# Kernel tuning notes

Measured on AMD Instinct MI355X. Metric: run time of the kernel, lower is better.

## Reference

```python
import jax, jax.numpy as jnp
import numpy as np

B, T, D, H = 2, 2048, 2048, 32
d = D // H  # head_dim = 64


def setup_inputs() -> dict:
    key = jax.random.key(0)
    ks = jax.random.split(key, 6)
    s = 2 ** (-2.5) * (2.0 / (D + D)) ** 0.5  # xavier_uniform-ish scale, gain 2^-2.5
    return {
        "hidden_states": jax.random.normal(ks[0], (B, T, D), jnp.float32),
        "Wq": jax.random.normal(ks[1], (D, D), jnp.float32) * s,
        "Wk": jax.random.normal(ks[2], (D, D), jnp.float32) * s,
        "Wv": jax.random.normal(ks[3], (D, D), jnp.float32) * s,
        "Wbeta": jax.random.normal(ks[4], (D, H), jnp.float32) * s,
        "b_beta": jnp.zeros((H,), jnp.float32),
        "Wo": jax.random.normal(ks[5], (D, D), jnp.float32) * s,
    }


def _l2norm(x):
    return x * jax.lax.rsqrt(jnp.sum(x * x, axis=-1, keepdims=True) + 1e-6)


def _parallel_hope(q, k, v, beta):
    """Householder delta-rule linear attention.
    q,k,v: [B,H,T,d]; beta: [B,H,T].
    Recurrence: S_t = S_{t-1} (I - beta_t k_t k_t^T) + beta_t k_t v_t^T  (k l2-normalized,
    so the update is a generalized Householder transform), o_t = q_t^T S_t.
    """
    q = _l2norm(q)
    k = _l2norm(k)

    def step(S, inp):
        q_t, k_t, v_t, b_t = inp  # [B,H,d], [B,H,d], [B,H,d], [B,H]
        # delta rule: new value replaces old prediction, gated by beta
        pred = jnp.einsum('bhk,bhkv->bhv', k_t, S)
        delta = (v_t - pred) * b_t[..., None]
        S = S + jnp.einsum('bhk,bhv->bhkv', k_t, delta)
        o_t = jnp.einsum('bhk,bhkv->bhv', q_t, S)
        return S, o_t

    S0 = jnp.zeros(q.shape[:2] + (q.shape[-1], v.shape[-1]), q.dtype)  # [B,H,d,d]
    xs = (jnp.moveaxis(q, 2, 0), jnp.moveaxis(k, 2, 0),
          jnp.moveaxis(v, 2, 0), jnp.moveaxis(beta, 2, 0))
    _, o = jax.lax.scan(step, S0, xs)  # [T,B,H,d]
    return jnp.moveaxis(o, 0, 2)  # [B,H,T,d]


def reference(hidden_states, Wq, Wk, Wv, Wbeta, b_beta, Wo):
    q = hidden_states @ Wq
    k = hidden_states @ Wk
    v = hidden_states @ Wv
    beta = jax.nn.sigmoid(hidden_states @ Wbeta + b_beta)  # [B,T,H]
    to_heads = lambda x: jnp.moveaxis(x.reshape(B, T, H, d), 1, 2)  # [B,H,T,d]
    q, k, v = to_heads(q), to_heads(k), to_heads(v)
    beta = jnp.moveaxis(beta, 1, 2)  # [B,H,T]
    o = _parallel_hope(q, k, v, beta)  # [B,H,T,d]
    o = jnp.moveaxis(o, 1, 2).reshape(B, T, D)
    return o @ Wo
```

## Files before the change

### kernel.cpp

```cpp
#include <hip/hip_runtime.h>
#include <hip/hip_bf16.h>

typedef __hip_bfloat16 bf16;
typedef __attribute__((ext_vector_type(8))) short short8;
typedef __attribute__((ext_vector_type(4))) float f32x4;

#define NB 2
#define NT 2048
#define ND 2048
#define NH 32
#define NM (NB*NT)
#define NCH 32

__global__ void detect_dtype(const unsigned short* __restrict__ hs, int* __restrict__ flag) {
  if (threadIdx.x == 0 && blockIdx.x == 0) {
    int cnt = 0;
    for (int i = 0; i < 2048; i += 2) {
      int e = (hs[i] >> 7) & 0xFF;
      if (e >= 141) ++cnt;
    }
    *flag = (cnt > 64) ? 1 : 0;
  }
}

__device__ __forceinline__ float loadf(const void* p, size_t i, int isf32) {
  return isf32 ? ((const float*)p)[i] : __bfloat162float(((const bf16*)p)[i]);
}

__global__ __launch_bounds__(256) void convert_bf16(const void* __restrict__ src,
                                                    bf16* __restrict__ dst,
                                                    long n, const int* __restrict__ flag) {
  const long i0 = ((long)blockIdx.x * 256 + threadIdx.x) * 8;
  if (i0 >= n) return;
  if (*flag) {
    const float* s = (const float*)src;
    #pragma unroll
    for (int j = 0; j < 8; ++j) dst[i0 + j] = __float2bfloat16(s[i0 + j]);
  } else {
    *(short8*)(dst + i0) = *(const short8*)((const bf16*)src + i0);
  }
}

__global__ __launch_bounds__(256) void transpose_cvt(const void* __restrict__ src,
                                                     bf16* __restrict__ dst,
                                                     int src_rows, int src_cols,
                                                     const int* __restrict__ flag) {
  __shared__ bf16 tile[64][65];
  const int f = *flag;
  const int tb_r = blockIdx.y * 64, tb_c = blockIdx.x * 64;
  const int tx = threadIdx.x & 63, ty = threadIdx.x >> 6;
  #pragma unroll
  for (int i = 0; i < 64; i += 4) {
    const int cc = tb_c + tx;
    tile[i + ty][tx] = (cc < src_cols)
      ? __float2bfloat16(loadf(src, (size_t)(tb_r + i + ty) * src_cols + cc, f))
      : __float2bfloat16(0.f);
  }
  __syncthreads();
  #pragma unroll
  for (int i = 0; i < 64; i += 4)
    dst[(size_t)(tb_c + i + ty) * src_rows + tb_r + tx] = tile[tx][i + ty];
}

__global__ __launch_bounds__(256) void transpose_qkvb(const void* __restrict__ Wq,
                                                      const void* __restrict__ Wk,
                                                      const void* __restrict__ Wv,
                                                      const void* __restrict__ Wb,
                                                      bf16* __restrict__ WT,
                                                      const int* __restrict__ flag) {
  __shared__ bf16 tile[64][65];
  const int z = blockIdx.z;
  if (z == 3 && blockIdx.x >= 2) return;
  const void* src = (z == 0) ? Wq : (z == 1) ? Wk : (z == 2) ? Wv : Wb;
  const int src_cols = (z == 3) ? 32 : 2048;
  bf16* dst = WT + (size_t)z * 2048 * 2048;
  const int f = *flag;
  const int tb_r = blockIdx.y * 64, tb_c = blockIdx.x * 64;
  const int tx = threadIdx.x & 63, ty = threadIdx.x >> 6;
  #pragma unroll
  for (int i = 0; i < 64; i += 4) {
    const int cc = tb_c + tx;
    tile[i + ty][tx] = (cc < src_cols)
      ? __float2bfloat16(loadf(src, (size_t)(tb_r + i + ty) * src_cols + cc, f))
      : __float2bfloat16(0.f);
  }
  __syncthreads();
  #pragma unroll
  for (int i = 0; i < 64; i += 4)
    dst[(size_t)(tb_c + i + ty) * 2048 + tb_r + tx] = tile[tx][i + ty];
}

__device__ __forceinline__ void gload_lds16(const void* g, void* l) {
  __builtin_amdgcn_global_load_lds((__attribute__((address_space(1))) const void*)g,
                                   (__attribute__((address_space(3))) void*)l,
                                   16, 0, 0);
}

__global__ __launch_bounds__(256) void gemm_bt(const bf16* __restrict__ A,
                                               const bf16* __restrict__ Bt,
                                               bf16* __restrict__ oq, bf16* __restrict__ ok2,
                                               bf16* __restrict__ ov, bf16* __restrict__ ob,
                                               void* __restrict__ outv,
                                               const int* __restrict__ outflag,
                                               int M, int K, int n_base) {
  __shared__ bf16 As[128 * 32];
  __shared__ bf16 Bs[128 * 32];
  const int tid = threadIdx.x;
  const int wave = tid >> 6, lane = tid & 63;
  const int m0 = blockIdx.y * 128, n0 = blockIdx.x * 128;
  const int wm = (wave >> 1) * 64, wn = (wave & 1) * 64;
  const int srow = lane >> 2, scol = (lane & 3) * 8;
  const int frow = lane & 15, fk = (lane >> 4) * 8;
  f32x4 acc[4][4] = {};

  for (int kb = 0; kb < K; kb += 32) {
    __syncthreads();
    #pragma unroll
    for (int j = 0; j < 2; ++j) {
      const int rbase = wave * 32 + j * 16;
      gload_lds16(A  + (size_t)(m0 + rbase + srow) * K + kb + scol, As + rbase * 32);
      gload_lds16(Bt + (size_t)(n0 + rbase + srow) * K + kb + scol, Bs + rbase * 32);
    }
    __syncthreads();
    short8 af[4], bfr[4];
    #pragma unroll
    for (int i = 0; i < 4; ++i)
      af[i] = *(const short8*)(As + (wm + i * 16 + frow) * 32 + fk);
    #pragma unroll
    for (int i = 0; i < 4; ++i)
      bfr[i] = *(const short8*)(Bs + (wn + i * 16 + frow) * 32 + fk);
    #pragma unroll
    for (int mi = 0; mi < 4; ++mi)
      #pragma unroll
      for (int ni = 0; ni < 4; ++ni)
        acc[mi][ni] = __builtin_amdgcn_mfma_f32_16x16x32_bf16(af[mi], bfr[ni], acc[mi][ni], 0, 0, 0);
  }

  const int crow = (lane >> 4) * 4, ccol = lane & 15;
  const int gn0 = n_base + n0;
  if (outflag) {
    const int f = *outflag;
    #pragma unroll
    for (int mi = 0; mi < 4; ++mi)
      #pragma unroll
      for (int ni = 0; ni < 4; ++ni)
        #pragma unroll
        for (int r = 0; r < 4; ++r) {
          const size_t idx = (size_t)(m0 + wm + mi * 16 + crow + r) * 2048 + gn0 + wn + ni * 16 + ccol;
          const float val = acc[mi][ni][r];
          if (f == 1) ((float*)outv)[idx] = val;
          else        ((bf16*)outv)[idx] = __float2bfloat16(val);
        }
  } else {
    const int seg = gn0 >> 11;
    bf16* o = (seg == 0) ? oq : (seg == 1) ? ok2 : (seg == 2) ? ov : ob;
    const int stride = (seg < 3) ? 2048 : 128;
    const int cb = (gn0 & 2047) + wn;
    if (seg <= 1) {
      #pragma unroll
      for (int mi = 0; mi < 4; ++mi)
        #pragma unroll
        for (int r = 0; r < 4; ++r) {
          float s = acc[mi][0][r] * acc[mi][0][r] + acc[mi][1][r] * acc[mi][1][r]
                  + acc[mi][2][r] * acc[mi][2][r] + acc[mi][3][r] * acc[mi][3][r];
          s += __shfl_xor(s, 1, 64); s += __shfl_xor(s, 2, 64);
          s += __shfl_xor(s, 4, 64); s += __shfl_xor(s, 8, 64);
          const float inv = rsqrtf(s + 1e-6f);
          #pragma unroll
          for (int ni = 0; ni < 4; ++ni) acc[mi][ni][r] *= inv;
        }
    }
    #pragma unroll
    for (int mi = 0; mi < 4; ++mi)
      #pragma unroll
      for (int ni = 0; ni < 4; ++ni)
        #pragma unroll
        for (int r = 0; r < 4; ++r)
          o[(size_t)(m0 + wm + mi * 16 + crow + r) * stride + cb + ni * 16 + ccol] =
            __float2bfloat16(acc[mi][ni][r]);
  }
}


template<int TB>
__device__ __forceinline__ void scan16(const float* __restrict__ Af,
                                       const bf16* __restrict__ vsrc,
                                       const float* __restrict__ Bsc,
                                       float (&u)[64], const int lane, const int wave,
                                       const float sgn,
                                       bf16* __restrict__ outT,
                                       bf16* __restrict__ gout) {
  constexpr int JM = (TB + 1) * 16;
  #pragma unroll
  for (int tt = 0; tt < 16; ++tt) {
    const int t = TB * 16 + tt;
    float pr0 = 0.f, pr1 = 0.f, pr2 = 0.f, pr3 = 0.f;
    #pragma unroll
    for (int i = 0; i < JM; i += 4) {
      const f32x4 a = *(const f32x4*)(Af + t * 64 + i);
      pr0 = __builtin_fmaf(a[0], u[i + 0], pr0);
      pr1 = __builtin_fmaf(a[1], u[i + 1], pr1);
      pr2 = __builtin_fmaf(a[2], u[i + 2], pr2);
      pr3 = __builtin_fmaf(a[3], u[i + 3], pr3);
    }
    const float ut = Bsc[t] * __bfloat162float(vsrc[t * 72 + lane])
                   - ((pr0 + pr1) + (pr2 + pr3));
    u[t] = ut;
    const bf16 sv = __float2bfloat16(sgn * ut);
    outT[lane * 72 + t] = sv;
    if (wave) gout[t * 64 + lane] = sv;
  }
}

__global__ __launch_bounds__(256) void chunk_scan(const bf16* __restrict__ k16,
                                                  bf16* __restrict__ v16,
                                                  const bf16* __restrict__ betab,
                                                  const void* __restrict__ bb,
                                                  const int* __restrict__ flag,
                                                  bf16* __restrict__ Gneg,
                                                  bf16* __restrict__ AcT,
                                                  bf16* __restrict__ Dc) {
  __shared__ bf16 Ks[64 * 72];
  __shared__ bf16 Vs[64 * 72];
  __shared__ bf16 GsT[64 * 72];
  __shared__ bf16 UsT[64 * 72];
  __shared__ float Af[64 * 64];
  __shared__ float Bsc[64];
  bf16* const KTs = (bf16*)Af;
  const int ch = blockIdx.x;
  const int c = ch & (NCH - 1), bh = ch >> 5;
  const int h = bh & (NH - 1), b = bh >> 5;
  const int tid = threadIdx.x, wave = tid >> 6, lane = tid & 63;
  const size_t rowb = ((size_t)b * NT + c * 64) * ND + (size_t)h * 64;

  short8 ktA0, ktB0, ktA1, ktB1;
  if (wave >= 2) {
    const int d0a = (wave - 2) * 16, d0b = d0a + 32;
    ktA0 = *(const short8*)(k16 + rowb + (size_t)lane * ND + d0a);
    ktB0 = *(const short8*)(k16 + rowb + (size_t)lane * ND + d0a + 8);
    ktA1 = *(const short8*)(k16 + rowb + (size_t)lane * ND + d0b);
    ktB1 = *(const short8*)(k16 + rowb + (size_t)lane * ND + d0b + 8);
  }
  {
    const int r0 = tid >> 3, sc = (tid & 7) * 8;
    #pragma unroll
    for (int rnd = 0; rnd < 2; ++rnd) {
      const int r = rnd * 32 + r0;
      *(short8*)(Ks + r * 72 + sc) = *(const short8*)(k16 + rowb + (size_t)r * ND + sc);
      *(short8*)(Vs + r * 72 + sc) = *(const short8*)(v16 + rowb + (size_t)r * ND + sc);
    }
  }
  if (tid < 64) {
    const float x = __bfloat162float(betab[((size_t)b * NT + c * 64 + tid) * 128 + h])
                    + loadf(bb, h, *flag);
    Bsc[tid] = 1.f / (1.f + expf(-x));
  }
  __syncthreads();

  const int frow = lane & 15, fk = (lane >> 4) * 8, cm = (lane >> 4) * 4;
  {
    short8 ma0 = *(const short8*)(Ks + (16 * wave + frow) * 72 + fk);
    short8 ma1 = *(const short8*)(Ks + (16 * wave + frow) * 72 + 32 + fk);
    #pragma unroll
    for (int n = 0; n < 4; ++n) {
      f32x4 m = {};
      m = __builtin_amdgcn_mfma_f32_16x16x32_bf16(ma0, *(const short8*)(Ks + (16 * n + frow) * 72 + fk), m, 0, 0, 0);
      m = __builtin_amdgcn_mfma_f32_16x16x32_bf16(ma1, *(const short8*)(Ks + (16 * n + frow) * 72 + 32 + fk), m, 0, 0, 0);
      #pragma unroll
      for (int r = 0; r < 4; ++r) {
        const int t = 16 * wave + cm + r, s = 16 * n + frow;
        Af[t * 64 + s] = (s < t) ? Bsc[t] * m[r] : 0.f;
      }
    }
  }
  __syncthreads();

  if (wave < 2) {
    float u[64];
    #pragma unroll
    for (int i = 0; i < 64; ++i) u[i] = 0.f;
    const bf16* vsrc = wave ? Ks : Vs;
    bf16* outT = wave ? GsT : UsT;
    bf16* gout = Gneg + (size_t)ch * 4096;
    const float sgn = wave ? -1.f : 1.f;
    scan16<0>(Af, vsrc, Bsc, u, lane, wave, sgn, outT, gout);
    scan16<1>(Af, vsrc, Bsc, u, lane, wave, sgn, outT, gout);
    scan16<2>(Af, vsrc, Bsc, u, lane, wave, sgn, outT, gout);
    scan16<3>(Af, vsrc, Bsc, u, lane, wave, sgn, outT, gout);
  }
  __syncthreads();

  if (wave >= 2) {
    const int d0a = (wave - 2) * 16, d0b = d0a + 32;
    #pragma unroll
    for (int j = 0; j < 8; ++j) {
      KTs[(d0a + j) * 72 + lane]     = ((const bf16*)&ktA0)[j];
      KTs[(d0a + 8 + j) * 72 + lane] = ((const bf16*)&ktB0)[j];
      KTs[(d0b + j) * 72 + lane]     = ((const bf16*)&ktA1)[j];
      KTs[(d0b + 8 + j) * 72 + lane] = ((const bf16*)&ktB1)[j];
    }
  }
  __syncthreads();

  short8 ka0 = *(const short8*)(KTs + (16 * wave + frow) * 72 + fk);
  short8 ka1 = *(const short8*)(KTs + (16 * wave + frow) * 72 + 32 + fk);
  short8 uu0 = *(const short8*)(UsT + (16 * wave + frow) * 72 + fk);
  short8 uu1 = *(const short8*)(UsT + (16 * wave + frow) * 72 + 32 + fk);
  #pragma unroll
  for (int n = 0; n < 4; ++n) {
    f32x4 aA = {}, aD = {};
    aA = __builtin_amdgcn_mfma_f32_16x16x32_bf16(ka0, *(const short8*)(GsT + (16 * n + frow) * 72 + fk), aA, 0, 0, 0);
    aA = __builtin_amdgcn_mfma_f32_16x16x32_bf16(ka1, *(const short8*)(GsT + (16 * n + frow) * 72 + 32 + fk), aA, 0, 0, 0);
    aD = __builtin_amdgcn_mfma_f32_16x16x32_bf16(uu0, *(const short8*)(KTs + (16 * n + frow) * 72 + fk), aD, 0, 0, 0);
    aD = __builtin_amdgcn_mfma_f32_16x16x32_bf16(uu1, *(const short8*)(KTs + (16 * n + frow) * 72 + 32 + fk), aD, 0, 0, 0);
    #pragma unroll
    for (int r = 0; r < 4; ++r) {
      Vs[(16 * wave + cm + r) * 64 + 16 * n + frow] = __float2bfloat16(aA[r]);
      Ks[(16 * wave + cm + r) * 64 + 16 * n + frow] = __float2bfloat16(aD[r]);
    }
  }
  __syncthreads();
  {
    const int r0 = tid >> 2, sc2 = (tid & 3) * 16;
    bf16* acg = AcT + (size_t)ch * 4096;
    bf16* dcg = Dc  + (size_t)ch * 4096;
    *(short8*)(acg + r0 * 64 + sc2)     = *(const short8*)(Vs + r0 * 64 + sc2);
    *(short8*)(acg + r0 * 64 + sc2 + 8) = *(const short8*)(Vs + r0 * 64 + sc2 + 8);
    *(short8*)(dcg + r0 * 64 + sc2)     = *(const short8*)(Ks + r0 * 64 + sc2);
    *(short8*)(dcg + r0 * 64 + sc2 + 8) = *(const short8*)(Ks + r0 * 64 + sc2 + 8);
    *(short8*)(v16 + rowb + (size_t)r0 * ND + sc2)     = *(const short8*)(UsT + r0 * 72 + sc2);
    *(short8*)(v16 + rowb + (size_t)r0 * ND + sc2 + 8) = *(const short8*)(UsT + r0 * 72 + sc2 + 8);
  }
}

__global__ __launch_bounds__(256) void state_seq(const bf16* __restrict__ AcT,
                                                 const bf16* __restrict__ Dc,
                                                 bf16* __restrict__ Sbuf) {
  __shared__ bf16 ST[64 * 72];
  const int bh = blockIdx.x;
  const int wave = threadIdx.x >> 6, lane = threadIdx.x & 63;
  const int frow = lane & 15, fk = (lane >> 4) * 8, cm = (lane >> 4) * 4;
  for (int i = threadIdx.x; i < 64 * 72 / 2; i += 256) ((unsigned int*)ST)[i] = 0u;
  f32x4 sacc[4] = {};
  const bf16* ac = AcT + (size_t)bh * NCH * 4096;
  const bf16* dc = Dc  + (size_t)bh * NCH * 4096;
  bf16* sb = Sbuf + (size_t)bh * NCH * 4096;
  #pragma unroll
  for (int n = 0; n < 4; ++n)
    #pragma unroll
    for (int r = 0; r < 4; ++r)
      sb[(16 * wave + cm + r) * 64 + 16 * n + frow] = __float2bfloat16(0.f);
  short8 bpre[4][2];
  float dpre[16];
  #pragma unroll
  for (int n = 0; n < 4; ++n) {
    bpre[n][0] = *(const short8*)(ac + (16 * n + frow) * 64 + fk);
    bpre[n][1] = *(const short8*)(ac + (16 * n + frow) * 64 + 32 + fk);
    #pragma unroll
    for (int r = 0; r < 4; ++r)
      dpre[n * 4 + r] = __bfloat162float(dc[(16 * wave + cm + r) * 64 + 16 * n + frow]);
  }
  __syncthreads();
  #pragma unroll 1
  for (int c = 0; c < NCH; ++c) {
    short8 a0 = *(const short8*)(ST + (16 * wave + frow) * 72 + fk);
    short8 a1 = *(const short8*)(ST + (16 * wave + frow) * 72 + 32 + fk);
    short8 bcur[4][2];
    float dcur[16];
    #pragma unroll
    for (int n = 0; n < 4; ++n) {
      bcur[n][0] = bpre[n][0]; bcur[n][1] = bpre[n][1];
      #pragma unroll
      for (int r = 0; r < 4; ++r) dcur[n * 4 + r] = dpre[n * 4 + r];
    }
    if (c + 1 < NCH) {
      const bf16* acn = ac + (size_t)(c + 1) * 4096;
      const bf16* dcn = dc + (size_t)(c + 1) * 4096;
      #pragma unroll
      for (int n = 0; n < 4; ++n) {
        bpre[n][0] = *(const short8*)(acn + (16 * n + frow) * 64 + fk);
        bpre[n][1] = *(const short8*)(acn + (16 * n + frow) * 64 + 32 + fk);
        #pragma unroll
        for (int r = 0; r < 4; ++r)
          dpre[n * 4 + r] = __bfloat162float(dcn[(16 * wave + cm + r) * 64 + 16 * n + frow]);
      }
    }
    #pragma unroll
    for (int n = 0; n < 4; ++n) {
      sacc[n] = __builtin_amdgcn_mfma_f32_16x16x32_bf16(a0, bcur[n][0], sacc[n], 0, 0, 0);
      sacc[n] = __builtin_amdgcn_mfma_f32_16x16x32_bf16(a1, bcur[n][1], sacc[n], 0, 0, 0);
      #pragma unroll
      for (int r = 0; r < 4; ++r) sacc[n][r] += dcur[n * 4 + r];
    }
    __syncthreads();
    #pragma unroll
    for (int n = 0; n < 4; ++n)
      #pragma unroll
      for (int r = 0; r < 4; ++r) {
        const bf16 sv = __float2bfloat16(sacc[n][r]);
        ST[(16 * wave + cm + r) * 72 + 16 * n + frow] = sv;
        if (c + 1 < NCH)
          sb[(size_t)(c + 1) * 4096 + (16 * wave + cm + r) * 64 + 16 * n + frow] = sv;
      }
    __syncthreads();
  }
}

__global__ __launch_bounds__(256) void chunk_out(bf16* __restrict__ q16,
                                                 const bf16* __restrict__ k16,
                                                 const bf16* __restrict__ v16,
                                                 const bf16* __restrict__ Gneg,
                                                 const bf16* __restrict__ Sbuf) {
  __shared__ bf16 UTs[64 * 72];
  __shared__ bf16 Pt[64 * 72];
  const int ch = blockIdx.x;
  const int c = ch & (NCH - 1), bh = ch >> 5;
  const int h = bh & (NH - 1), b = bh >> 5;
  const int tid = threadIdx.x, wave = tid >> 6, lane = tid & 63;
  const int frow = lane & 15, fk = (lane >> 4) * 8, cm = (lane >> 4) * 4;
  const size_t qkb = ((size_t)b * NT + c * 64) * ND + (size_t)h * 64;
  const bf16* Sb = Sbuf + (size_t)ch * 4096;
  const bf16* Gc = Gneg + (size_t)ch * 4096;
  {
    const int r0 = tid >> 2, sc2 = (tid & 3) * 16;
    *(short8*)(UTs + r0 * 72 + sc2)     = *(const short8*)(v16 + qkb + (size_t)r0 * ND + sc2);
    *(short8*)(UTs + r0 * 72 + sc2 + 8) = *(const short8*)(v16 + qkb + (size_t)r0 * ND + sc2 + 8);
  }
  short8 qa0 = *(const short8*)(q16 + qkb + (size_t)(16 * wave + frow) * ND + fk);
  short8 qa1 = *(const short8*)(q16 + qkb + (size_t)(16 * wave + frow) * ND + 32 + fk);
  f32x4 pacc[4];
  #pragma unroll
  for (int n = 0; n < 4; ++n) {
    f32x4 a = {};
    a = __builtin_amdgcn_mfma_f32_16x16x32_bf16(qa0, *(const short8*)(k16 + qkb + (size_t)(16 * n + frow) * ND + fk), a, 0, 0, 0);
    a = __builtin_amdgcn_mfma_f32_16x16x32_bf16(qa1, *(const short8*)(k16 + qkb + (size_t)(16 * n + frow) * ND + 32 + fk), a, 0, 0, 0);
    pacc[n] = a;
  }
  __syncthreads();
  f32x4 uacc[4];
  #pragma unroll
  for (int n = 0; n < 4; ++n)
    #pragma unroll
    for (int r = 0; r < 4; ++r)
      uacc[n][r] = __bfloat162float(UTs[(16 * wave + cm + r) * 72 + 16 * n + frow]);
  #pragma unroll
  for (int n = 0; n < 4; ++n)
    #pragma unroll
    for (int r = 0; r < 4; ++r) {
      const int mg = 16 * wave + cm + r, ng = 16 * n + frow;
      Pt[mg * 72 + ng] = __float2bfloat16(ng <= mg ? pacc[n][r] : 0.f);
    }
  short8 sa0 = *(const short8*)(Sb + (16 * wave + frow) * 64 + fk);
  short8 sa1 = *(const short8*)(Sb + (16 * wave + frow) * 64 + 32 + fk);
  #pragma unroll
  for (int n = 0; n < 4; ++n) {
    uacc[n] = __builtin_amdgcn_mfma_f32_16x16x32_bf16(sa0, *(const short8*)(Gc + (16 * n + frow) * 64 + fk), uacc[n], 0, 0, 0);
    uacc[n] = __builtin_amdgcn_mfma_f32_16x16x32_bf16(sa1, *(const short8*)(Gc + (16 * n + frow) * 64 + 32 + fk), uacc[n], 0, 0, 0);
  }
  __syncthreads();
  #pragma unroll
  for (int n = 0; n < 4; ++n)
    #pragma unroll
    for (int r = 0; r < 4; ++r)
      UTs[(16 * wave + cm + r) * 72 + 16 * n + frow] = __float2bfloat16(uacc[n][r]);
  __syncthreads();
  short8 pa0 = *(const short8*)(Pt + (16 * wave + frow) * 72 + fk);
  short8 pa1 = *(const short8*)(Pt + (16 * wave + frow) * 72 + 32 + fk);
  #pragma unroll
  for (int n = 0; n < 4; ++n) {
    f32x4 o = {};
    o = __builtin_amdgcn_mfma_f32_16x16x32_bf16(qa0, *(const short8*)(Sb + (16 * n + frow) * 64 + fk), o, 0, 0, 0);
    o = __builtin_amdgcn_mfma_f32_16x16x32_bf16(qa1, *(const short8*)(Sb + (16 * n + frow) * 64 + 32 + fk), o, 0, 0, 0);
    o = __builtin_amdgcn_mfma_f32_16x16x32_bf16(pa0, *(const short8*)(UTs + (16 * n + frow) * 72 + fk), o, 0, 0, 0);
    o = __builtin_amdgcn_mfma_f32_16x16x32_bf16(pa1, *(const short8*)(UTs + (16 * n + frow) * 72 + 32 + fk), o, 0, 0, 0);
    #pragma unroll
    for (int r = 0; r < 4; ++r)
      q16[qkb + (size_t)(16 * wave + cm + r) * ND + 16 * n + frow] = __float2bfloat16(o[r]);
  }
}


__global__ __launch_bounds__(128) void chunk_scan_c(const bf16* __restrict__ k16,
                                                    bf16* __restrict__ v16,
                                                    const bf16* __restrict__ betab,
                                                    const void* __restrict__ bb,
                                                    const int* __restrict__ flag,
                                                    bf16* __restrict__ Gneg) {
  __shared__ bf16 Ks[64 * 64];
  __shared__ bf16 Vs[64 * 64];
  __shared__ bf16 Gs[64 * 64];
  __shared__ float Bs[64];
  const int ch = blockIdx.x;
  const int c = ch & (NCH - 1), bh = ch >> 5;
  const int h = bh & (NH - 1), b = bh >> 5;
  const int tid = threadIdx.x;
  const int wave = tid >> 6, lane = tid & 63;
  const size_t rowb = ((size_t)b * NT + c * 64) * ND + (size_t)h * 64;
  const int sr = tid >> 3, sc = (tid & 7) * 8;
  #pragma unroll
  for (int rnd = 0; rnd < 4; ++rnd) {
    const int r = rnd * 16 + sr;
    *(short8*)(Ks + r * 64 + sc) = *(const short8*)(k16 + rowb + (size_t)r * ND + sc);
    *(short8*)(Vs + r * 64 + sc) = *(const short8*)(v16 + rowb + (size_t)r * ND + sc);
  }
  if (tid < 64) {
    const float x = __bfloat162float(betab[((size_t)b * NT + c * 64 + tid) * 128 + h])
                    + loadf(bb, h, *flag);
    Bs[tid] = 1.f / (1.f + expf(-x));
  }
  __syncthreads();
  float S[64];
  #pragma unroll
  for (int i = 0; i < 64; ++i) S[i] = 0.f;
  const bf16* val_src = wave ? Ks : Vs;
  #pragma unroll 1
  for (int t = 0; t < 64; ++t) {
    uint4 ku[8];
    #pragma unroll
    for (int i = 0; i < 8; ++i) ku[i] = ((const uint4*)(Ks + t * 64))[i];
    const float val = __bfloat162float(val_src[t * 64 + lane]);
    const float bt = Bs[t];
    float kvf[64];
    #pragma unroll
    for (int i = 0; i < 8; ++i) {
      kvf[8*i+0] = __uint_as_float(ku[i].x << 16);
      kvf[8*i+1] = __uint_as_float(ku[i].x & 0xffff0000u);
      kvf[8*i+2] = __uint_as_float(ku[i].y << 16);
      kvf[8*i+3] = __uint_as_float(ku[i].y & 0xffff0000u);
      kvf[8*i+4] = __uint_as_float(ku[i].z << 16);
      kvf[8*i+5] = __uint_as_float(ku[i].z & 0xffff0000u);
      kvf[8*i+6] = __uint_as_float(ku[i].w << 16);
      kvf[8*i+7] = __uint_as_float(ku[i].w & 0xffff0000u);
    }
    float p0 = 0, p1 = 0, p2 = 0, p3 = 0;
    #pragma unroll
    for (int i = 0; i < 16; ++i) {
      p0 += kvf[4*i+0] * S[4*i+0];
      p1 += kvf[4*i+1] * S[4*i+1];
      p2 += kvf[4*i+2] * S[4*i+2];
      p3 += kvf[4*i+3] * S[4*i+3];
    }
    const float u = bt * (val - ((p0 + p1) + (p2 + p3)));
    #pragma unroll
    for (int i = 0; i < 16; ++i) {
      S[4*i+0] += kvf[4*i+0] * u;
      S[4*i+1] += kvf[4*i+1] * u;
      S[4*i+2] += kvf[4*i+2] * u;
      S[4*i+3] += kvf[4*i+3] * u;
    }
    if (wave) Gs[t * 64 + lane] = __float2bfloat16(-u);
    else      Vs[t * 64 + lane] = __float2bfloat16(u);
  }
  __syncthreads();
  bf16* gout = Gneg + (size_t)ch * 4096;
  #pragma unroll
  for (int rnd = 0; rnd < 4; ++rnd) {
    const int r = rnd * 16 + sr;
    *(short8*)(v16 + rowb + (size_t)r * ND + sc) = *(const short8*)(Vs + r * 64 + sc);
    *(short8*)(gout + r * 64 + sc)               = *(const short8*)(Gs + r * 64 + sc);
  }
}

__global__ __launch_bounds__(256) void chunk_seq_mono(bf16* q16,
                                                      const bf16* __restrict__ k16,
                                                      const bf16* __restrict__ Ul,
                                                      const bf16* __restrict__ Gneg) {
  __shared__ bf16 ST[64 * 72];
  __shared__ bf16 Ubt[64 * 72];
  __shared__ bf16 Pt[64 * 72];
  __shared__ bf16 KTl[64 * 72];
  const int bh = blockIdx.x, h = bh & (NH - 1), b = bh >> 5;
  const int wave = threadIdx.x >> 6, lane = threadIdx.x & 63;
  const int frow = lane & 15, q4 = lane >> 4, fk = q4 * 8;
  const int cm = q4 * 4;
  for (int i = threadIdx.x; i < 64 * 72 / 2; i += 256) ((unsigned int*)ST)[i] = 0u;
  __syncthreads();
  f32x4 sacc[4] = {};
  #pragma unroll 1
  for (int c = 0; c < NCH; ++c) {
    const bf16* Gc = Gneg + ((size_t)bh * NCH + c) * 4096;
    const size_t qkb = ((size_t)b * NT + c * 64) * ND + (size_t)h * 64;
    {
      short8 r0 = *(const short8*)(k16 + qkb + (size_t)lane * ND + 16 * wave);
      short8 r1 = *(const short8*)(k16 + qkb + (size_t)lane * ND + 16 * wave + 8);
      #pragma unroll
      for (int j = 0; j < 8; ++j) {
        KTl[(16 * wave + j) * 72 + lane]     = ((const bf16*)&r0)[j];
        KTl[(16 * wave + 8 + j) * 72 + lane] = ((const bf16*)&r1)[j];
      }
    }
    short8 ga0 = *(const short8*)(Gc + (16 * wave + frow) * 64 + fk);
    short8 ga1 = *(const short8*)(Gc + (16 * wave + frow) * 64 + 32 + fk);
    #pragma unroll
    for (int n = 0; n < 4; ++n) {
      f32x4 acc;
      #pragma unroll
      for (int r = 0; r < 4; ++r)
        acc[r] = __bfloat162float(Ul[qkb + (size_t)(16 * wave + cm + r) * ND + 16 * n + frow]);
      acc = __builtin_amdgcn_mfma_f32_16x16x32_bf16(ga0, *(const short8*)(ST + (16 * n + frow) * 72 + fk), acc, 0, 0, 0);
      acc = __builtin_amdgcn_mfma_f32_16x16x32_bf16(ga1, *(const short8*)(ST + (16 * n + frow) * 72 + 32 + fk), acc, 0, 0, 0);
      #pragma unroll
      for (int r = 0; r < 4; ++r)
        Ubt[(16 * n + frow) * 72 + 16 * wave + cm + r] = __float2bfloat16(acc[r]);
    }
    __syncthreads();
    short8 qa0 = *(const short8*)(q16 + qkb + (size_t)(16 * wave + frow) * ND + fk);
    short8 qa1 = *(const short8*)(q16 + qkb + (size_t)(16 * wave + frow) * ND + 32 + fk);
    #pragma unroll
    for (int n = 0; n < 4; ++n) {
      f32x4 acc = {};
      acc = __builtin_amdgcn_mfma_f32_16x16x32_bf16(qa0, *(const short8*)(k16 + qkb + (size_t)(16 * n + frow) * ND + fk), acc, 0, 0, 0);
      acc = __builtin_amdgcn_mfma_f32_16x16x32_bf16(qa1, *(const short8*)(k16 + qkb + (size_t)(16 * n + frow) * ND + 32 + fk), acc, 0, 0, 0);
      #pragma unroll
      for (int r = 0; r < 4; ++r) {
        const int mg = 16 * wave + cm + r, ng = 16 * n + frow;
        Pt[mg * 72 + ng] = __float2bfloat16(ng <= mg ? acc[r] : 0.f);
      }
    }
    __syncthreads();
    short8 pa0 = *(const short8*)(Pt + (16 * wave + frow) * 72 + fk);
    short8 pa1 = *(const short8*)(Pt + (16 * wave + frow) * 72 + 32 + fk);
    #pragma unroll
    for (int n = 0; n < 4; ++n) {
      f32x4 acc = {};
      acc = __builtin_amdgcn_mfma_f32_16x16x32_bf16(qa0, *(const short8*)(ST + (16 * n + frow) * 72 + fk), acc, 0, 0, 0);
      acc = __builtin_amdgcn_mfma_f32_16x16x32_bf16(qa1, *(const short8*)(ST + (16 * n + frow) * 72 + 32 + fk), acc, 0, 0, 0);
      acc = __builtin_amdgcn_mfma_f32_16x16x32_bf16(pa0, *(const short8*)(Ubt + (16 * n + frow) * 72 + fk), acc, 0, 0, 0);
      acc = __builtin_amdgcn_mfma_f32_16x16x32_bf16(pa1, *(const short8*)(Ubt + (16 * n + frow) * 72 + 32 + fk), acc, 0, 0, 0);
      #pragma unroll
      for (int r = 0; r < 4; ++r)
        q16[qkb + (size_t)(16 * wave + cm + r) * ND + 16 * n + frow] = __float2bfloat16(acc[r]);
    }
    __syncthreads();
    short8 ua0 = *(const short8*)(Ubt + (16 * wave + frow) * 72 + fk);
    short8 ua1 = *(const short8*)(Ubt + (16 * wave + frow) * 72 + 32 + fk);
    #pragma unroll
    for (int n = 0; n < 4; ++n) {
      sacc[n] = __builtin_amdgcn_mfma_f32_16x16x32_bf16(ua0, *(const short8*)(KTl + (16 * n + frow) * 72 + fk), sacc[n], 0, 0, 0);
      sacc[n] = __builtin_amdgcn_mfma_f32_16x16x32_bf16(ua1, *(const short8*)(KTl + (16 * n + frow) * 72 + 32 + fk), sacc[n], 0, 0, 0);
      #pragma unroll
      for (int r = 0; r < 4; ++r)
        ST[(16 * wave + cm + r) * 72 + 16 * n + frow] = __float2bfloat16(sacc[n][r]);
    }
    __syncthreads();
  }
}

extern "C" void kernel_launch(void* const* d_in, const int* in_sizes, int n_in,
                              void* d_out, int out_size, void* d_ws, size_t ws_size,
                              hipStream_t stream) {
  const void* hs = d_in[0];
  const void* Wq = d_in[1];
  const void* Wk = d_in[2];
  const void* Wv = d_in[3];
  const void* Wb = d_in[4];
  const void* bb = d_in[5];
  const void* Wo = d_in[6];

  char* ws = (char*)d_ws;
  size_t off = 0;
  auto alloc = [&](size_t bytes) {
    void* p = ws + off;
    off += (bytes + 255) & ~(size_t)255;
    return p;
  };
  const size_t szW = (size_t)6272 * 2048 * 2;
  const size_t szM = (size_t)NM * ND * 2;
  const size_t szB = (size_t)NM * 128 * 2;
  const size_t need_fused = 512 + szW + 4 * szM + szB + 2 * szM;

  if (ws_size >= need_fused) {
    int*  flag  = (int*) alloc(256);
    bf16* WT    = (bf16*)alloc(szW);
    bf16* hs16  = (bf16*)alloc(szM);
    bf16* q16   = (bf16*)alloc(szM);
    bf16* k16   = (bf16*)alloc(szM);
    bf16* v16   = (bf16*)alloc(szM);
    bf16* betab = (bf16*)alloc(szB);
    bf16* AcT   = (bf16*)alloc(szM);
    bf16* Dc    = (bf16*)alloc(szM);
    bf16* Gneg  = WT;
    bf16* WoT   = WT + (size_t)8 * 1024 * 1024;
    bf16* Sbuf  = hs16;

    detect_dtype<<<1, 64, 0, stream>>>((const unsigned short*)hs, flag);
    convert_bf16<<<(NM * ND) / (256 * 8), 256, 0, stream>>>(hs, hs16, (long)NM * ND, flag);

    transpose_qkvb<<<dim3(32, 32, 4), 256, 0, stream>>>(Wq, Wk, Wv, Wb, WT, flag);
    gemm_bt<<<dim3(49, 32), 256, 0, stream>>>(hs16, WT, q16, k16, v16, betab,
                                              nullptr, nullptr, NM, ND, 0);

    chunk_scan<<<NB * NH * NCH, 256, 0, stream>>>(k16, v16, betab, bb, flag, Gneg, AcT, Dc);
    state_seq<<<NB * NH, 256, 0, stream>>>(AcT, Dc, Sbuf);
    chunk_out<<<NB * NH * NCH, 256, 0, stream>>>(q16, k16, v16, Gneg, Sbuf);

    transpose_cvt<<<dim3(32, 32), 256, 0, stream>>>(Wo, WoT, 2048, 2048, flag);
    gemm_bt<<<dim3(16, 32), 256, 0, stream>>>(q16, WoT, nullptr, nullptr, nullptr, nullptr,
                                              d_out, flag, NM, ND, 0);
  } else {
    int*  flag  = (int*) alloc(256);
    bf16* Wt    = (bf16*)alloc((size_t)2048 * 2048 * 2);
    bf16* hs16  = (bf16*)alloc(szM);
    bf16* q16   = (bf16*)alloc(szM);
    bf16* k16   = (bf16*)alloc(szM);
    bf16* v16   = (bf16*)alloc(szM);
    bf16* betab = (bf16*)alloc(szB);
    bf16* Gneg  = hs16;

    detect_dtype<<<1, 64, 0, stream>>>((const unsigned short*)hs, flag);
    convert_bf16<<<(NM * ND) / (256 * 8), 256, 0, stream>>>(hs, hs16, (long)NM * ND, flag);

    transpose_cvt<<<dim3(32, 32), 256, 0, stream>>>(Wq, Wt, 2048, 2048, flag);
    gemm_bt<<<dim3(16, 32), 256, 0, stream>>>(hs16, Wt, q16, k16, v16, betab, nullptr, nullptr, NM, ND, 0);
    transpose_cvt<<<dim3(32, 32), 256, 0, stream>>>(Wk, Wt, 2048, 2048, flag);
    gemm_bt<<<dim3(16, 32), 256, 0, stream>>>(hs16, Wt, q16, k16, v16, betab, nullptr, nullptr, NM, ND, 2048);
    transpose_cvt<<<dim3(32, 32), 256, 0, stream>>>(Wv, Wt, 2048, 2048, flag);
    gemm_bt<<<dim3(16, 32), 256, 0, stream>>>(hs16, Wt, q16, k16, v16, betab, nullptr, nullptr, NM, ND, 4096);
    transpose_cvt<<<dim3(2, 32),  256, 0, stream>>>(Wb, Wt, 2048, 32, flag);
    gemm_bt<<<dim3(1, 32), 256, 0, stream>>>(hs16, Wt, q16, k16, v16, betab, nullptr, nullptr, NM, ND, 6144);

    chunk_scan_c<<<NB * NH * NCH, 128, 0, stream>>>(k16, v16, betab, bb, flag, Gneg);
    chunk_seq_mono<<<NB * NH, 256, 0, stream>>>(q16, k16, v16, Gneg);

    transpose_cvt<<<dim3(32, 32), 256, 0, stream>>>(Wo, Wt, 2048, 2048, flag);
    gemm_bt<<<dim3(16, 32), 256, 0, stream>>>(q16, Wt, nullptr, nullptr, nullptr, nullptr,
                                              d_out, flag, NM, ND, 0);
  }
}
```

Baseline: 575.7 us.

## Add 256x256-tile pipelined GEMM for fused QKV/beta projection

Replaces the QKV+beta projection GEMM with a new 512-thread kernel using 256x256 output tiles, double-buffered direct-to-LDS global loads, swizzled LDS layout, wave priority phases and an XCD-aware block remap. Beta output is padded to 256 columns, so the beta weight transpose now covers more blocks and the readers use the new stride. Workspace is also repacked so AcT aliases the weight buffer. The larger tiles aim to raise arithmetic intensity and hide load latency, at the cost of higher register and LDS pressure and some wasted padded beta columns.

```diff
diff --git a/kernel.cpp b/kernel.cpp
--- a/kernel.cpp
+++ b/kernel.cpp
@@ -70,7 +70,7 @@
                                                       const int* __restrict__ flag) {
   __shared__ bf16 tile[64][65];
   const int z = blockIdx.z;
-  if (z == 3 && blockIdx.x >= 2) return;
+  if (z == 3 && blockIdx.x >= 4) return;
   const void* src = (z == 0) ? Wq : (z == 1) ? Wk : (z == 2) ? Wv : Wb;
   const int src_cols = (z == 3) ? 32 : 2048;
   bf16* dst = WT + (size_t)z * 2048 * 2048;
@@ -179,6 +179,145 @@
           o[(size_t)(m0 + wm + mi * 16 + crow + r) * stride + cb + ni * 16 + ccol] =
             __float2bfloat16(acc[mi][ni][r]);
   }
+}
+
+
+#define MFMA_Q(MB, NB_)                                                          \
+  _Pragma("unroll") for (int mi2 = 0; mi2 < 4; ++mi2) {                          \
+    _Pragma("unroll") for (int ni2 = 0; ni2 < 2; ++ni2) {                        \
+      acc[(MB) + mi2][(NB_) + ni2] = __builtin_amdgcn_mfma_f32_16x16x32_bf16(    \
+          aF[(MB) + mi2][0], bF[ni2][0], acc[(MB) + mi2][(NB_) + ni2], 0, 0, 0); \
+      acc[(MB) + mi2][(NB_) + ni2] = __builtin_amdgcn_mfma_f32_16x16x32_bf16(    \
+          aF[(MB) + mi2][1], bF[ni2][1], acc[(MB) + mi2][(NB_) + ni2], 0, 0, 0); \
+    } }
+
+#define READ_B(NBASE)                                                            \
+  _Pragma("unroll") for (int ni2 = 0; ni2 < 2; ++ni2)                            \
+    _Pragma("unroll") for (int kk = 0; kk < 2; ++kk)                             \
+      bF[ni2][kk] = *(const short8*)((const char*)lB +                           \
+        (brow0 + ((NBASE) + ni2) * 16 + frow) * 128 + kk * 64 + fcol);
+
+#define PH_OPEN() do { __builtin_amdgcn_s_barrier();                             \
+  asm volatile("s_waitcnt lgkmcnt(0)" ::: "memory");                             \
+  __builtin_amdgcn_sched_barrier(0);                                             \
+  __builtin_amdgcn_s_setprio(1); } while (0)
+
+#define PH_CLOSE() do { __builtin_amdgcn_s_setprio(0);                           \
+  __builtin_amdgcn_s_barrier(); } while (0)
+
+__global__ __launch_bounds__(512, 2) void gemm256(const bf16* __restrict__ A,
+                                                  const bf16* __restrict__ Bt,
+                                                  bf16* __restrict__ oq, bf16* __restrict__ ok2,
+                                                  bf16* __restrict__ ov, bf16* __restrict__ ob,
+                                                  int K, int ntn) {
+  __shared__ bf16 LA[2][2][8192];
+  __shared__ bf16 LB[2][2][8192];
+  const int tid = threadIdx.x;
+  const int wave = tid >> 6, lane = tid & 63;
+  const int wm = wave >> 2, wn = wave & 3;
+  const int frow = lane & 15, fq = lane >> 4;
+  const int cpx = (int)gridDim.x >> 3;
+  const int wg = ((int)blockIdx.x & 7) * cpx + ((int)blockIdx.x >> 3);
+  const int mtile = wg / ntn, ntile = wg % ntn;
+  const int m0 = mtile * 256, n0 = ntile * 256;
+  const int NTK = K >> 6;
+  const int fcol = (fq * 16) ^ (((frow >> 2) & 1) << 5);
+  int srow[2], scolb[2];
+  #pragma unroll
+  for (int j = 0; j < 2; ++j) {
+    const int q = wave * 1024 + j * 8192 + lane * 16;
+    const int qs = q ^ (((q >> 9) & 1) << 5);
+    srow[j] = qs >> 7;
+    scolb[j] = (qs & 127) >> 1;
+  }
+  const int lofs = wave * 1024;
+
+  f32x4 acc[8][4] = {};
+
+  auto STAGE = [&](const bf16* __restrict__ G, int row0, int kcol, bf16* lhalf) {
+    #pragma unroll
+    for (int j = 0; j < 2; ++j)
+      gload_lds16(G + (size_t)(row0 + srow[j]) * K + kcol + scolb[j],
+                  (char*)lhalf + lofs + j * 8192);
+  };
+
+  STAGE(A,  m0,       0,  LA[0][0]);
+  STAGE(A,  m0 + 128, 0,  LA[0][1]);
+  STAGE(Bt, n0,       0,  LB[0][0]);
+  STAGE(Bt, n0 + 128, 0,  LB[0][1]);
+  STAGE(A,  m0,       64, LA[1][0]);
+  STAGE(A,  m0 + 128, 64, LA[1][1]);
+  asm volatile("s_waitcnt vmcnt(4)" ::: "memory");
+  __builtin_amdgcn_s_barrier();
+
+  const int brow0 = (wn & 1) * 64;
+  #pragma unroll 1
+  for (int t = 0; t < NTK; ++t) {
+    const int par = t & 1;
+    const bf16* lA = LA[par][wm];
+    const bf16* lB = LB[par][wn >> 1];
+    short8 aF[8][2], bF[2][2];
+    #pragma unroll
+    for (int mi = 0; mi < 8; ++mi)
+      #pragma unroll
+      for (int kk = 0; kk < 2; ++kk)
+        aF[mi][kk] = *(const short8*)((const char*)lA + (mi * 16 + frow) * 128 + kk * 64 + fcol);
+    READ_B(0)
+    if (t + 1 < NTK) STAGE(Bt, n0, (t + 1) * 64, LB[par ^ 1][0]);
+    PH_OPEN();
+    MFMA_Q(0, 0)
+    PH_CLOSE();
+    READ_B(2)
+    if (t + 1 < NTK) STAGE(Bt, n0 + 128, (t + 1) * 64, LB[par ^ 1][1]);
+    if (t + 2 < NTK) STAGE(A, m0, (t + 2) * 64, LA[par][0]);
+    PH_OPEN();
+    MFMA_Q(0, 2)
+    PH_CLOSE();
+    READ_B(0)
+    if (t + 2 < NTK) STAGE(A, m0 + 128, (t + 2) * 64, LA[par][1]);
+    PH_OPEN();
+    MFMA_Q(4, 0)
+    PH_CLOSE();
+    READ_B(2)
+    PH_OPEN();
+    MFMA_Q(4, 2)
+    __builtin_amdgcn_s_setprio(0);
+    if (t + 1 < NTK) {
+      if (t == NTK - 2) asm volatile("s_waitcnt vmcnt(0)" ::: "memory");
+      else              asm volatile("s_waitcnt vmcnt(4)" ::: "memory");
+      __builtin_amdgcn_s_barrier();
+    }
+  }
+
+  const int crow = fq * 4, ccol = frow;
+  const int gn0w = n0 + wn * 64;
+  const int seg = gn0w >> 11;
+  bf16* o = (seg == 0) ? oq : (seg == 1) ? ok2 : (seg == 2) ? ov : ob;
+  const int stride = (seg < 3) ? 2048 : 256;
+  const int cb = (seg < 3) ? (gn0w & 2047) : (gn0w - 6144);
+  if (seg <= 1) {
+    #pragma unroll
+    for (int mi = 0; mi < 8; ++mi)
+      #pragma unroll
+      for (int r = 0; r < 4; ++r) {
+        float s = acc[mi][0][r] * acc[mi][0][r] + acc[mi][1][r] * acc[mi][1][r]
+                + acc[mi][2][r] * acc[mi][2][r] + acc[mi][3][r] * acc[mi][3][r];
+        s += __shfl_xor(s, 1, 64); s += __shfl_xor(s, 2, 64);
+        s += __shfl_xor(s, 4, 64); s += __shfl_xor(s, 8, 64);
+        const float inv = rsqrtf(s + 1e-6f);
+        #pragma unroll
+        for (int ni = 0; ni < 4; ++ni) acc[mi][ni][r] *= inv;
+      }
+  }
+  const int rowb = m0 + wm * 128;
+  #pragma unroll
+  for (int mi = 0; mi < 8; ++mi)
+    #pragma unroll
+    for (int ni = 0; ni < 4; ++ni)
+      #pragma unroll
+      for (int r = 0; r < 4; ++r)
+        o[(size_t)(rowb + mi * 16 + crow + r) * stride + cb + ni * 16 + ccol] =
+          __float2bfloat16(acc[mi][ni][r]);
 }
 
 
@@ -251,7 +390,7 @@
     }
   }
   if (tid < 64) {
-    const float x = __bfloat162float(betab[((size_t)b * NT + c * 64 + tid) * 128 + h])
+    const float x = __bfloat162float(betab[((size_t)b * NT + c * 64 + tid) * 256 + h])
                     + loadf(bb, h, *flag);
     Bsc[tid] = 1.f / (1.f + expf(-x));
   }
@@ -664,31 +803,31 @@
     off += (bytes + 255) & ~(size_t)255;
     return p;
   };
-  const size_t szW = (size_t)6272 * 2048 * 2;
-  const size_t szM = (size_t)NM * ND * 2;
-  const size_t szB = (size_t)NM * 128 * 2;
-  const size_t need_fused = 512 + szW + 4 * szM + szB + 2 * szM;
+  const size_t szW2 = (size_t)32 * 1024 * 1024;
+  const size_t szM  = (size_t)NM * ND * 2;
+  const size_t szB2 = (size_t)NM * 256 * 2;
+  const size_t szB  = (size_t)NM * 128 * 2;
+  const size_t need_fused = 512 + szW2 + 4 * szM + szB2 + szM;
 
   if (ws_size >= need_fused) {
     int*  flag  = (int*) alloc(256);
-    bf16* WT    = (bf16*)alloc(szW);
+    bf16* WT    = (bf16*)alloc(szW2);
     bf16* hs16  = (bf16*)alloc(szM);
     bf16* q16   = (bf16*)alloc(szM);
     bf16* k16   = (bf16*)alloc(szM);
     bf16* v16   = (bf16*)alloc(szM);
-    bf16* betab = (bf16*)alloc(szB);
-    bf16* AcT   = (bf16*)alloc(szM);
+    bf16* betab = (bf16*)alloc(szB2);
     bf16* Dc    = (bf16*)alloc(szM);
     bf16* Gneg  = WT;
-    bf16* WoT   = WT + (size_t)8 * 1024 * 1024;
+    bf16* AcT   = WT + (size_t)8 * 1024 * 1024;
+    bf16* WoT   = AcT;
     bf16* Sbuf  = hs16;
 
     detect_dtype<<<1, 64, 0, stream>>>((const unsigned short*)hs, flag);
     convert_bf16<<<(NM * ND) / (256 * 8), 256, 0, stream>>>(hs, hs16, (long)NM * ND, flag);
 
     transpose_qkvb<<<dim3(32, 32, 4), 256, 0, stream>>>(Wq, Wk, Wv, Wb, WT, flag);
-    gemm_bt<<<dim3(49, 32), 256, 0, stream>>>(hs16, WT, q16, k16, v16, betab,
-                                              nullptr, nullptr, NM, ND, 0);
+    gemm256<<<400, 512, 0, stream>>>(hs16, WT, q16, k16, v16, betab, ND, 25);
 
     chunk_scan<<<NB * NH * NCH, 256, 0, stream>>>(k16, v16, betab, bb, flag, Gneg, AcT, Dc);
     state_seq<<<NB * NH, 256, 0, stream>>>(AcT, Dc, Sbuf);
```

Result: slower. 588.7 us (+2.2%).

## Add 128x256-tile gemm128 kernel with XCD-aware tile mapping for projections

Applied to the files above, without the earlier changes.

Introduces a new 512-thread GEMM kernel with 128x256 output tiles, double-buffered direct global-to-LDS loads and swizzled LDS addressing. It replaces gemm_bt for both the fused QKV/beta projection and the output projection. A custom blockIdx remap groups tiles by XCD for L2 reuse. The beta segment is padded to 256 columns, with the consumer stride and workspace layout (AcT aliased into WT) adjusted to match. This aims to raise MFMA utilisation and cut global traffic per FLOP, but it adds aliasing risk in the workspace reuse.

```diff
diff --git a/kernel.cpp b/kernel.cpp
--- a/kernel.cpp
+++ b/kernel.cpp
@@ -70,7 +70,7 @@
                                                       const int* __restrict__ flag) {
   __shared__ bf16 tile[64][65];
   const int z = blockIdx.z;
-  if (z == 3 && blockIdx.x >= 2) return;
+  if (z == 3 && blockIdx.x >= 4) return;
   const void* src = (z == 0) ? Wq : (z == 1) ? Wk : (z == 2) ? Wv : Wb;
   const int src_cols = (z == 3) ? 32 : 2048;
   bf16* dst = WT + (size_t)z * 2048 * 2048;
@@ -179,6 +179,123 @@
           o[(size_t)(m0 + wm + mi * 16 + crow + r) * stride + cb + ni * 16 + ccol] =
             __float2bfloat16(acc[mi][ni][r]);
   }
+}
+
+__global__ __launch_bounds__(512, 4) void gemm128(const bf16* __restrict__ A,
+                                                  const bf16* __restrict__ Bt,
+                                                  bf16* __restrict__ oq, bf16* __restrict__ ok2,
+                                                  bf16* __restrict__ ov, bf16* __restrict__ ob,
+                                                  void* __restrict__ outv,
+                                                  const int* __restrict__ outflag,
+                                                  int K, int ntn) {
+  __shared__ __align__(16) bf16 LA[2][128 * 32];
+  __shared__ __align__(16) bf16 LB[2][256 * 32];
+  const int tid = threadIdx.x;
+  const int wave = tid >> 6, lane = tid & 63;
+  const int wm = wave >> 2, wn = wave & 3;
+  const int frow = lane & 15, fq = lane >> 4;
+  int mtile, ntile;
+  if (ntn == 25) {
+    const int x = (int)blockIdx.x & 7, r = (int)blockIdx.x >> 3;
+    const int mg = x >> 2, ng = x & 3;
+    if (ng == 0)      { mtile = mg * 16 + (r & 15);  ntile = r >> 4; }
+    else if (r < 96)  { mtile = mg * 16 + (r & 15);  ntile = 1 + ng * 6 + (r >> 4); }
+    else { const int r2 = 100 + (ng - 1) * 4 + (r - 96);
+           mtile = mg * 16 + (r2 & 15); ntile = r2 >> 4; }
+  } else {
+    const int cpx = (int)gridDim.x >> 3;
+    const int wg = ((int)blockIdx.x & 7) * cpx + ((int)blockIdx.x >> 3);
+    mtile = wg / ntn; ntile = wg % ntn;
+  }
+  const int m0 = mtile * 128, n0 = ntile * 256;
+  const int NTK = K >> 5;
+  const int fcol = (fq * 16) ^ ((frow & 3) << 4);
+  const int q  = tid * 16;
+  const int qs = q ^ (((q >> 6) & 3) << 4);
+  const int sr = qs >> 6;
+  const int sc = (qs & 63) >> 1;
+  const int wofs = wave * 1024;
+
+  f32x4 acc[4][4] = {};
+
+  #define STAGE128(T, BUF)                                                          \
+    do { const int kc = (T) * 32;                                                   \
+      gload_lds16(A  + (size_t)(m0 + sr) * K + kc + sc,       (char*)LA[BUF] + wofs);\
+      gload_lds16(Bt + (size_t)(n0 + sr) * K + kc + sc,       (char*)LB[BUF] + wofs);\
+      gload_lds16(Bt + (size_t)(n0 + 128 + sr) * K + kc + sc, (char*)LB[BUF] + 8192 + wofs);\
+    } while (0)
+
+  STAGE128(0, 0);
+  asm volatile("s_waitcnt vmcnt(0)" ::: "memory");
+  __syncthreads();
+
+  #pragma unroll 1
+  for (int t = 0; t < NTK; ++t) {
+    const int cur = t & 1;
+    if (t + 1 < NTK) STAGE128(t + 1, cur ^ 1);
+    const char* lA = (const char*)LA[cur];
+    const char* lB = (const char*)LB[cur];
+    short8 af[4], bfr[4];
+    #pragma unroll
+    for (int i = 0; i < 4; ++i)
+      af[i] = *(const short8*)(lA + (wm * 64 + i * 16 + frow) * 64 + fcol);
+    #pragma unroll
+    for (int i = 0; i < 4; ++i)
+      bfr[i] = *(const short8*)(lB + (wn * 64 + i * 16 + frow) * 64 + fcol);
+    #pragma unroll
+    for (int mi = 0; mi < 4; ++mi)
+      #pragma unroll
+      for (int ni = 0; ni < 4; ++ni)
+        acc[mi][ni] = __builtin_amdgcn_mfma_f32_16x16x32_bf16(af[mi], bfr[ni], acc[mi][ni], 0, 0, 0);
+    __syncthreads();
+  }
+  #undef STAGE128
+
+  const int crow = fq * 4, ccol = frow;
+  const int rowb = m0 + wm * 64;
+  if (outv) {
+    const int f = *outflag;
+    const int cb = n0 + wn * 64;
+    #pragma unroll
+    for (int mi = 0; mi < 4; ++mi)
+      #pragma unroll
+      for (int ni = 0; ni < 4; ++ni)
+        #pragma unroll
+        for (int r = 0; r < 4; ++r) {
+          const size_t idx = (size_t)(rowb + mi * 16 + crow + r) * 2048 + cb + ni * 16 + ccol;
+          const float val = acc[mi][ni][r];
+          if (f == 1) ((float*)outv)[idx] = val;
+          else        ((bf16*)outv)[idx] = __float2bfloat16(val);
+        }
+    return;
+  }
+  const int gn0w = n0 + wn * 64;
+  const int seg = gn0w >> 11;
+  bf16* o = (seg == 0) ? oq : (seg == 1) ? ok2 : (seg == 2) ? ov : ob;
+  const int stride = (seg < 3) ? 2048 : 256;
+  const int cb = (seg < 3) ? (gn0w & 2047) : (gn0w - 6144);
+  if (seg <= 1) {
+    #pragma unroll
+    for (int mi = 0; mi < 4; ++mi)
+      #pragma unroll
+      for (int r = 0; r < 4; ++r) {
+        float s = acc[mi][0][r] * acc[mi][0][r] + acc[mi][1][r] * acc[mi][1][r]
+                + acc[mi][2][r] * acc[mi][2][r] + acc[mi][3][r] * acc[mi][3][r];
+        s += __shfl_xor(s, 1, 64); s += __shfl_xor(s, 2, 64);
+        s += __shfl_xor(s, 4, 64); s += __shfl_xor(s, 8, 64);
+        const float inv = rsqrtf(s + 1e-6f);
+        #pragma unroll
+        for (int ni = 0; ni < 4; ++ni) acc[mi][ni][r] *= inv;
+      }
+  }
+  #pragma unroll
+  for (int mi = 0; mi < 4; ++mi)
+    #pragma unroll
+    for (int ni = 0; ni < 4; ++ni)
+      #pragma unroll
+      for (int r = 0; r < 4; ++r)
+        o[(size_t)(rowb + mi * 16 + crow + r) * stride + cb + ni * 16 + ccol] =
+          __float2bfloat16(acc[mi][ni][r]);
 }
 
 
@@ -251,7 +368,7 @@
     }
   }
   if (tid < 64) {
-    const float x = __bfloat162float(betab[((size_t)b * NT + c * 64 + tid) * 128 + h])
+    const float x = __bfloat162float(betab[((size_t)b * NT + c * 64 + tid) * 256 + h])
                     + loadf(bb, h, *flag);
     Bsc[tid] = 1.f / (1.f + expf(-x));
   }
@@ -664,39 +781,40 @@
     off += (bytes + 255) & ~(size_t)255;
     return p;
   };
-  const size_t szW = (size_t)6272 * 2048 * 2;
-  const size_t szM = (size_t)NM * ND * 2;
-  const size_t szB = (size_t)NM * 128 * 2;
-  const size_t need_fused = 512 + szW + 4 * szM + szB + 2 * szM;
+  const size_t szW2 = (size_t)32 * 1024 * 1024;
+  const size_t szM  = (size_t)NM * ND * 2;
+  const size_t szB2 = (size_t)NM * 256 * 2;
+  const size_t szB  = (size_t)NM * 128 * 2;
+  const size_t need_fused = 512 + szW2 + 4 * szM + szB2 + szM;
 
   if (ws_size >= need_fused) {
     int*  flag  = (int*) alloc(256);
-    bf16* WT    = (bf16*)alloc(szW);
+    bf16* WT    = (bf16*)alloc(szW2);
     bf16* hs16  = (bf16*)alloc(szM);
     bf16* q16   = (bf16*)alloc(szM);
     bf16* k16   = (bf16*)alloc(szM);
     bf16* v16   = (bf16*)alloc(szM);
-    bf16* betab = (bf16*)alloc(szB);
-    bf16* AcT   = (bf16*)alloc(szM);
+    bf16* betab = (bf16*)alloc(szB2);
     bf16* Dc    = (bf16*)alloc(szM);
     bf16* Gneg  = WT;
-    bf16* WoT   = WT + (size_t)8 * 1024 * 1024;
+    bf16* AcT   = WT + (size_t)8 * 1024 * 1024;
+    bf16* WoT   = AcT;
     bf16* Sbuf  = hs16;
 
     detect_dtype<<<1, 64, 0, stream>>>((const unsigned short*)hs, flag);
     convert_bf16<<<(NM * ND) / (256 * 8), 256, 0, stream>>>(hs, hs16, (long)NM * ND, flag);
 
     transpose_qkvb<<<dim3(32, 32, 4), 256, 0, stream>>>(Wq, Wk, Wv, Wb, WT, flag);
-    gemm_bt<<<dim3(49, 32), 256, 0, stream>>>(hs16, WT, q16, k16, v16, betab,
-                                              nullptr, nullptr, NM, ND, 0);
+    gemm128<<<800, 512, 0, stream>>>(hs16, WT, q16, k16, v16, betab,
+                                     nullptr, nullptr, ND, 25);
 
     chunk_scan<<<NB * NH * NCH, 256, 0, stream>>>(k16, v16, betab, bb, flag, Gneg, AcT, Dc);
     state_seq<<<NB * NH, 256, 0, stream>>>(AcT, Dc, Sbuf);
     chunk_out<<<NB * NH * NCH, 256, 0, stream>>>(q16, k16, v16, Gneg, Sbuf);
 
     transpose_cvt<<<dim3(32, 32), 256, 0, stream>>>(Wo, WoT, 2048, 2048, flag);
-    gemm_bt<<<dim3(16, 32), 256, 0, stream>>>(q16, WoT, nullptr, nullptr, nullptr, nullptr,
-                                              d_out, flag, NM, ND, 0);
+    gemm128<<<256, 512, 0, stream>>>(q16, WoT, nullptr, nullptr, nullptr, nullptr,
+                                     d_out, flag, ND, 8);
   } else {
     int*  flag  = (int*) alloc(256);
     bf16* Wt    = (bf16*)alloc((size_t)2048 * 2048 * 2);
```

Result: faster. 552.4 us (-4.1%).
